# Performance work log

Measured on AMD Instinct MI355X. Metric: run time of the kernel, lower is better.

## Reference

```python
import jax, jax.numpy as jnp
import numpy as np

DIM = 256
HEADS = 8
DIM_FF = 1024
N = 4096
HEAD_DIM = DIM // HEADS
SCALE = HEAD_DIM ** -0.5


def layer_norm(x, gamma, beta, eps=1e-5):
    mu = jnp.mean(x, axis=-1, keepdims=True)
    var = jnp.var(x, axis=-1, keepdims=True)
    return (x - mu) * jax.lax.rsqrt(var + eps) * gamma + beta


def setup_inputs() -> dict:
    key = jax.random.key(0)
    ks = jax.random.split(key, 8)
    x = jax.random.normal(ks[0], (N, DIM), dtype=jnp.float32)
    adj = jax.random.randint(ks[1], (N, N), 0, 2, dtype=jnp.int32)
    adj = adj.at[jnp.arange(N), jnp.arange(N)].set(1)  # self-loops
    s = 1.0 / np.sqrt(DIM)
    w_qkv = jax.random.normal(ks[2], (DIM, 3 * DIM), dtype=jnp.float32) * s
    w_proj = jax.random.normal(ks[3], (DIM, DIM), dtype=jnp.float32) * s
    b_proj = jnp.zeros((DIM,), jnp.float32)
    w1 = jax.random.normal(ks[4], (DIM, DIM_FF), dtype=jnp.float32) * s
    b1 = jnp.zeros((DIM_FF,), jnp.float32)
    w2 = jax.random.normal(ks[5], (DIM_FF, DIM), dtype=jnp.float32) / np.sqrt(DIM_FF)
    b2 = jnp.zeros((DIM,), jnp.float32)
    g1 = jnp.ones((DIM,), jnp.float32)
    be1 = jnp.zeros((DIM,), jnp.float32)
    g2 = jnp.ones((DIM,), jnp.float32)
    be2 = jnp.zeros((DIM,), jnp.float32)
    return {"x": x, "adj": adj, "w_qkv": w_qkv, "w_proj": w_proj,
            "b_proj": b_proj, "w1": w1, "b1": b1, "w2": w2, "b2": b2,
            "g1": g1, "be1": be1, "g2": g2, "be2": be2}


def reference(x, adj, w_qkv, w_proj, b_proj, w1, b1, w2, b2, g1, be1, g2, be2):
    n = x.shape[0]
    qkv = layer_norm(x, g1, be1) @ w_qkv            # (N, 3*dim)
    qkv = qkv.reshape(n, 3, HEADS, HEAD_DIM)
    q, k, v = qkv[:, 0], qkv[:, 1], qkv[:, 2]       # (N, h, d)
    scores = jnp.einsum('nhd,mhd->hnm', q, k) * SCALE
    mask = (adj != 0)[None, :, :]                    # (1, N, N)
    scores = jnp.where(mask, scores, -jnp.inf)
    attn = jax.nn.softmax(scores, axis=-1)           # (h, N, N)
    out = jnp.einsum('hnm,mhd->nhd', attn, v).reshape(n, DIM)
    x = x + out @ w_proj + b_proj
    h2 = layer_norm(x, g2, be2)
    ff = jax.nn.gelu(h2 @ w1 + b1) @ w2 + b2
    return x + ff
```

## Files before the change

### kernel.cpp

```cpp
#include <hip/hip_runtime.h>
#include <hip/hip_bf16.h>

#define NT 4096
#define DM 256
#define NH 8
#define HD 32
#define DFF 1024

typedef __attribute__((ext_vector_type(8))) short s8v;
typedef __attribute__((ext_vector_type(4))) float f4v;
typedef __attribute__((ext_vector_type(2))) float f2v;
typedef __attribute__((ext_vector_type(16))) float f16v;
typedef __attribute__((ext_vector_type(4))) int i4v;

static __device__ __forceinline__ unsigned short f2b(float f){
  union{float f; unsigned u;} v; v.f=f;
  return (unsigned short)((v.u + 0x7FFFu + ((v.u>>16)&1u))>>16);
}

static __device__ __forceinline__ void gl_lds16(const void* g, void* l){
  __builtin_amdgcn_global_load_lds(
      (const __attribute__((address_space(1))) unsigned int*)g,
      (__attribute__((address_space(3))) unsigned int*)l, 16, 0, 0);
}

__global__ __launch_bounds__(256) void prologue_kernel(
    const int* __restrict__ adj, unsigned long long* __restrict__ mask,
    const float* __restrict__ wqkv, const float* __restrict__ wproj,
    const float* __restrict__ w1, const float* __restrict__ w2,
    unsigned short* __restrict__ wqkvT, unsigned short* __restrict__ wprojT,
    unsigned short* __restrict__ w1T, unsigned short* __restrict__ w2T,
    const float* __restrict__ x, const float* __restrict__ g1,
    const float* __restrict__ be1, unsigned short* __restrict__ h1){
  int bx = blockIdx.x;
  if (bx < 1024){
    int wv = threadIdx.x>>6, lane = threadIdx.x&63;
    int base = (bx*4 + wv)*64;
    for (int it=0; it<16; ++it){
      int w0 = base + it*4;
      unsigned long long b0 = __ballot(adj[(long)(w0+0)*64 + lane]!=0);
      unsigned long long b1 = __ballot(adj[(long)(w0+1)*64 + lane]!=0);
      unsigned long long b2 = __ballot(adj[(long)(w0+2)*64 + lane]!=0);
      unsigned long long b3 = __ballot(adj[(long)(w0+3)*64 + lane]!=0);
      if (lane==0){ mask[w0]=b0; mask[w0+1]=b1; mask[w0+2]=b2; mask[w0+3]=b3; }
    }
  } else if (bx < 1152){
    int t = (bx-1024)*256 + threadIdx.x;
    const int stride = 128*256;
    for (int i=t;i<768*DM;i+=stride){int n=i>>8,k=i&255; wqkvT[i]=f2b(wqkv[k*768+n]);}
    for (int i=t;i<DM*DM;i+=stride){int n=i>>8,k=i&255; wprojT[i]=f2b(wproj[k*DM+n]);}
    for (int i=t;i<DFF*DM;i+=stride){int n=i>>8,k=i&255; w1T[i]=f2b(w1[k*DFF+n]);}
    for (int i=t;i<DM*DFF;i+=stride){int n=i/DFF,k=i-n*DFF; w2T[i]=f2b(w2[k*DM+n]);}
  } else {
    int wv = threadIdx.x>>6, lane = threadIdx.x&63;
    int rbase = (bx-1152)*4 + wv;
    for (int j=0;j<8;j++){
      int row = rbase + j*512;
      float4 v = *(const float4*)(x + row*DM + lane*4);
      float s = v.x+v.y+v.z+v.w;
      float sq = v.x*v.x+v.y*v.y+v.z*v.z+v.w*v.w;
      #pragma unroll
      for (int m=1;m<64;m<<=1){ s += __shfl_xor(s,m); sq += __shfl_xor(sq,m); }
      float mu = s*(1.0f/DM);
      float rs = rsqrtf(sq*(1.0f/DM) - mu*mu + 1e-5f);
      float4 gv = *(const float4*)(g1 + lane*4);
      float4 bv = *(const float4*)(be1 + lane*4);
      ushort4 o;
      o.x = f2b((v.x-mu)*rs*gv.x + bv.x);
      o.y = f2b((v.y-mu)*rs*gv.y + bv.y);
      o.z = f2b((v.z-mu)*rs*gv.z + bv.z);
      o.w = f2b((v.w-mu)*rs*gv.w + bv.w);
      *(ushort4*)(h1 + row*DM + lane*4) = o;
    }
  }
}

template<int KD, int MODE>
__global__ __launch_bounds__(256,4) void gemm24(const unsigned short* __restrict__ A,
            const unsigned short* __restrict__ Wt, const float* __restrict__ bias,
            void* __restrict__ outp,
            unsigned short* __restrict__ Qp, unsigned short* __restrict__ Kp,
            unsigned short* __restrict__ Vt){
  int wv = threadIdx.x>>6, lane = threadIdx.x&63;
  int lo = lane&15, hi = lane>>4;
  int r0 = blockIdx.y*32;
  int cbase = blockIdx.x*256 + wv*16;
  const unsigned short* ar0 = A + (r0+lo)*KD + hi*8;
  const unsigned short* ar1 = ar0 + 16*KD;
  const unsigned short* br0 = Wt + (cbase     +lo)*KD + hi*8;
  const unsigned short* br1 = Wt + (cbase+ 64 +lo)*KD + hi*8;
  const unsigned short* br2 = Wt + (cbase+128 +lo)*KD + hi*8;
  const unsigned short* br3 = Wt + (cbase+192 +lo)*KD + hi*8;
  f4v c00={0,0,0,0},c01={0,0,0,0},c02={0,0,0,0},c03={0,0,0,0};
  f4v c10={0,0,0,0},c11={0,0,0,0},c12={0,0,0,0},c13={0,0,0,0};
  #pragma unroll 2
  for (int k0=0;k0<KD;k0+=32){
    s8v a0 = *(const s8v*)(ar0 + k0);
    s8v a1 = *(const s8v*)(ar1 + k0);
    s8v b0 = *(const s8v*)(br0 + k0);
    s8v b1 = *(const s8v*)(br1 + k0);
    s8v b2 = *(const s8v*)(br2 + k0);
    s8v b3 = *(const s8v*)(br3 + k0);
    c00 = __builtin_amdgcn_mfma_f32_16x16x32_bf16(a0,b0,c00,0,0,0);
    c10 = __builtin_amdgcn_mfma_f32_16x16x32_bf16(a1,b0,c10,0,0,0);
    c01 = __builtin_amdgcn_mfma_f32_16x16x32_bf16(a0,b1,c01,0,0,0);
    c11 = __builtin_amdgcn_mfma_f32_16x16x32_bf16(a1,b1,c11,0,0,0);
    c02 = __builtin_amdgcn_mfma_f32_16x16x32_bf16(a0,b2,c02,0,0,0);
    c12 = __builtin_amdgcn_mfma_f32_16x16x32_bf16(a1,b2,c12,0,0,0);
    c03 = __builtin_amdgcn_mfma_f32_16x16x32_bf16(a0,b3,c03,0,0,0);
    c13 = __builtin_amdgcn_mfma_f32_16x16x32_bf16(a1,b3,c13,0,0,0);
  }
  const float scl2 = (float)(0.17677669529663687 * 1.4426950408889634);
  #pragma unroll
  for (int rt=0;rt<2;rt++){
    f4v e0 = rt? c10:c00, e1 = rt? c11:c01, e2 = rt? c12:c02, e3 = rt? c13:c03;
    int nb = r0 + rt*16 + hi*4;
    #pragma unroll
    for (int jj=0;jj<4;jj++){
      f4v acc = jj==0?e0 : jj==1?e1 : jj==2?e2 : e3;
      int c = cbase + jj*64 + lo;
      if (MODE==0){
        int which = c>>8, hd = c&255, hh = hd>>5, d = hd&31;
        #pragma unroll
        for (int r=0;r<4;r++){
          int n = nb + r;
          float val = acc[r];
          if (which==0) Qp[(hh*NT+n)*HD+d]=f2b(val*scl2);
          else if (which==1) Kp[(hh*NT+n)*HD+d]=f2b(val);
          else Vt[(hh*HD+d)*NT+n]=f2b(val);
        }
      }
    }
  }
}

__global__ __launch_bounds__(512,2) void attn_kernel(
    const unsigned short* __restrict__ Q, const unsigned short* __restrict__ K,
    const unsigned short* __restrict__ Vt, const unsigned* __restrict__ mb32,
    unsigned short* __restrict__ out){
  __shared__ float Opart[8][32][34];
  __shared__ float llS[8][32];
  int wv = threadIdx.x>>6, lane = threadIdx.x&63;
  int l31 = lane&31, hi5 = lane>>5;
  int h = blockIdx.x, q0 = blockIdx.y*64;
  const unsigned short* QbA = Q + (h*NT + q0 + l31)*HD + hi5*8;
  const unsigned short* QbB = QbA + 32*HD;
  s8v bqA1 = *(const s8v*)(QbA);
  s8v bqA2 = *(const s8v*)(QbA + 16);
  s8v bqB1 = *(const s8v*)(QbB);
  s8v bqB2 = *(const s8v*)(QbB + 16);
  const unsigned short* Kb = K + h*NT*HD;
  const unsigned short* Vb = Vt + (h*HD + l31)*NT;
  const unsigned* mrowA = mb32 + (q0+l31)*(NT/32) + wv*16;
  const unsigned* mrowB = mrowA + 32*(NT/32);
  const float C0 = -11.541560327111707f;
  const f16v c0v = {C0,C0,C0,C0,C0,C0,C0,C0,C0,C0,C0,C0,C0,C0,C0,C0};
  f2v lacA = {0.f,0.f}, lacB = {0.f,0.f};
  f16v accA = {0,0,0,0,0,0,0,0,0,0,0,0,0,0,0,0};
  f16v accB = {0,0,0,0,0,0,0,0,0,0,0,0,0,0,0,0};
  union SU { f16v v; f2v p[8]; };
  const unsigned short* Kt0 = Kb + (wv*512 + l31)*HD + hi5*8;
  s8v kc1 = *(const s8v*)(Kt0);
  s8v kc2 = *(const s8v*)(Kt0 + 16);
  for (int tg=0; tg<4; tg++){
    i4v mw4A = *(const i4v*)(mrowA + tg*4);
    i4v mw4B = *(const i4v*)(mrowB + tg*4);
    #pragma unroll
    for (int ti=0; ti<4; ti++){
      int t = tg*4 + ti;
      int m0 = wv*512 + t*32;
      const unsigned short* Vtp = Vb + m0 + hi5*8;
      s8v av1 = *(const s8v*)(Vtp);
      s8v av2 = *(const s8v*)(Vtp + 16);
      int tn = (t<15)? t+1 : 15;
      const unsigned short* Ktn = Kb + (wv*512 + tn*32 + l31)*HD + hi5*8;
      s8v kn1 = *(const s8v*)(Ktn);
      s8v kn2 = *(const s8v*)(Ktn + 16);
      SU sa, sb;
      __builtin_amdgcn_s_setprio(1);
      sa.v = __builtin_amdgcn_mfma_f32_32x32x16_bf16(kc1, bqA1, c0v, 0,0,0);
      sa.v = __builtin_amdgcn_mfma_f32_32x32x16_bf16(kc2, bqA2, sa.v, 0,0,0);
      sb.v = __builtin_amdgcn_mfma_f32_32x32x16_bf16(kc1, bqB1, c0v, 0,0,0);
      sb.v = __builtin_amdgcn_mfma_f32_32x32x16_bf16(kc2, bqB2, sb.v, 0,0,0);
      __builtin_amdgcn_s_setprio(0);
      unsigned mwA = ((unsigned)mw4A[ti]) >> (4*hi5);
      unsigned mwB = ((unsigned)mw4B[ti]) >> (4*hi5);
      #pragma unroll
      for (int r=0;r<16;r++){
        int bp = (r&3)+8*(r>>2);
        float pa = __builtin_amdgcn_exp2f(sa.v[r]);
        float pb = __builtin_amdgcn_exp2f(sb.v[r]);
        sa.v[r] = ((mwA >> bp) & 1u) ? pa : 0.0f;
        sb.v[r] = ((mwB >> bp) & 1u) ? pb : 0.0f;
      }
      #pragma unroll
      for (int i=0;i<8;i++){ lacA += sa.p[i]; lacB += sb.p[i]; }
      unsigned a0,a1,a2,a3,a4,a5,a6,a7, b0,b1,b2,b3,b4,b5,b6,b7;
      asm("v_cvt_pk_bf16_f32 %0, %1, %2" : "=v"(a0) : "v"(sa.v[0]),  "v"(sa.v[1]));
      asm("v_cvt_pk_bf16_f32 %0, %1, %2" : "=v"(a1) : "v"(sa.v[2]),  "v"(sa.v[3]));
      asm("v_cvt_pk_bf16_f32 %0, %1, %2" : "=v"(a2) : "v"(sa.v[4]),  "v"(sa.v[5]));
      asm("v_cvt_pk_bf16_f32 %0, %1, %2" : "=v"(a3) : "v"(sa.v[6]),  "v"(sa.v[7]));
      asm("v_cvt_pk_bf16_f32 %0, %1, %2" : "=v"(a4) : "v"(sa.v[8]),  "v"(sa.v[9]));
      asm("v_cvt_pk_bf16_f32 %0, %1, %2" : "=v"(a5) : "v"(sa.v[10]), "v"(sa.v[11]));
      asm("v_cvt_pk_bf16_f32 %0, %1, %2" : "=v"(a6) : "v"(sa.v[12]), "v"(sa.v[13]));
      asm("v_cvt_pk_bf16_f32 %0, %1, %2" : "=v"(a7) : "v"(sa.v[14]), "v"(sa.v[15]));
      asm("v_permlane32_swap_b32 %0, %1" : "+v"(a0), "+v"(a2));
      asm("v_permlane32_swap_b32 %0, %1" : "+v"(a1), "+v"(a3));
      asm("v_permlane32_swap_b32 %0, %1" : "+v"(a4), "+v"(a6));
      asm("v_permlane32_swap_b32 %0, %1" : "+v"(a5), "+v"(a7));
      asm("v_cvt_pk_bf16_f32 %0, %1, %2" : "=v"(b0) : "v"(sb.v[0]),  "v"(sb.v[1]));
      asm("v_cvt_pk_bf16_f32 %0, %1, %2" : "=v"(b1) : "v"(sb.v[2]),  "v"(sb.v[3]));
      asm("v_cvt_pk_bf16_f32 %0, %1, %2" : "=v"(b2) : "v"(sb.v[4]),  "v"(sb.v[5]));
      asm("v_cvt_pk_bf16_f32 %0, %1, %2" : "=v"(b3) : "v"(sb.v[6]),  "v"(sb.v[7]));
      asm("v_cvt_pk_bf16_f32 %0, %1, %2" : "=v"(b4) : "v"(sb.v[8]),  "v"(sb.v[9]));
      asm("v_cvt_pk_bf16_f32 %0, %1, %2" : "=v"(b5) : "v"(sb.v[10]), "v"(sb.v[11]));
      asm("v_cvt_pk_bf16_f32 %0, %1, %2" : "=v"(b6) : "v"(sb.v[12]), "v"(sb.v[13]));
      asm("v_cvt_pk_bf16_f32 %0, %1, %2" : "=v"(b7) : "v"(sb.v[14]), "v"(sb.v[15]));
      asm("v_permlane32_swap_b32 %0, %1" : "+v"(b0), "+v"(b2));
      asm("v_permlane32_swap_b32 %0, %1" : "+v"(b1), "+v"(b3));
      asm("v_permlane32_swap_b32 %0, %1" : "+v"(b4), "+v"(b6));
      asm("v_permlane32_swap_b32 %0, %1" : "+v"(b5), "+v"(b7));
      i4v pA1i = {(int)a0,(int)a1,(int)a2,(int)a3};
      i4v pA2i = {(int)a4,(int)a5,(int)a6,(int)a7};
      i4v pB1i = {(int)b0,(int)b1,(int)b2,(int)b3};
      i4v pB2i = {(int)b4,(int)b5,(int)b6,(int)b7};
      s8v pA1 = __builtin_bit_cast(s8v, pA1i);
      s8v pA2 = __builtin_bit_cast(s8v, pA2i);
      s8v pB1 = __builtin_bit_cast(s8v, pB1i);
      s8v pB2 = __builtin_bit_cast(s8v, pB2i);
      __builtin_amdgcn_s_setprio(1);
      accA = __builtin_amdgcn_mfma_f32_32x32x16_bf16(av1, pA1, accA, 0,0,0);
      accA = __builtin_amdgcn_mfma_f32_32x32x16_bf16(av2, pA2, accA, 0,0,0);
      accB = __builtin_amdgcn_mfma_f32_32x32x16_bf16(av1, pB1, accB, 0,0,0);
      accB = __builtin_amdgcn_mfma_f32_32x32x16_bf16(av2, pB2, accB, 0,0,0);
      __builtin_amdgcn_s_setprio(0);
      kc1 = kn1; kc2 = kn2;
    }
  }
  int tid = threadIdx.x;
  int qq = tid>>4, dd = 2*(tid&15);
  #pragma unroll
  for (int i=0;i<8;i++){
    int d = (2*i&3) + 8*(i>>1) + 4*hi5;
    float2 p2; p2.x = accA[2*i]; p2.y = accA[2*i+1];
    *(float2*)&Opart[wv][l31][d] = p2;
  }
  float lsumA = lacA[0] + lacA[1];
  lsumA += __shfl_xor(lsumA, 32);
  if (hi5==0) llS[wv][l31] = lsumA;
  __syncthreads();
  {
    float L=0.f, o0=0.f, o1=0.f;
    #pragma unroll
    for (int u=0;u<8;u++){
      L  += llS[u][qq];
      o0 += Opart[u][qq][dd];
      o1 += Opart[u][qq][dd+1];
    }
    float inv = 1.0f/L;
    float r0 = o0*inv, r1 = o1*inv;
    unsigned pw;
    asm("v_cvt_pk_bf16_f32 %0, %1, %2" : "=v"(pw) : "v"(r0), "v"(r1));
    *(unsigned*)(out + (q0+qq)*DM + h*HD + dd) = pw;
  }
  __syncthreads();
  #pragma unroll
  for (int i=0;i<8;i++){
    int d = (2*i&3) + 8*(i>>1) + 4*hi5;
    float2 p2; p2.x = accB[2*i]; p2.y = accB[2*i+1];
    *(float2*)&Opart[wv][l31][d] = p2;
  }
  float lsumB = lacB[0] + lacB[1];
  lsumB += __shfl_xor(lsumB, 32);
  if (hi5==0) llS[wv][l31] = lsumB;
  __syncthreads();
  {
    float L=0.f, o0=0.f, o1=0.f;
    #pragma unroll
    for (int u=0;u<8;u++){
      L  += llS[u][qq];
      o0 += Opart[u][qq][dd];
      o1 += Opart[u][qq][dd+1];
    }
    float inv = 1.0f/L;
    float r0 = o0*inv, r1 = o1*inv;
    unsigned pw;
    asm("v_cvt_pk_bf16_f32 %0, %1, %2" : "=v"(pw) : "v"(r0), "v"(r1));
    *(unsigned*)(out + (q0+32+qq)*DM + h*HD + dd) = pw;
  }
}

__global__ __launch_bounds__(512,2) void tail_kernel(
    const unsigned short* __restrict__ ao, const unsigned short* __restrict__ wprojT,
    const float* __restrict__ bproj, const float* __restrict__ x,
    const float* __restrict__ g2, const float* __restrict__ be2,
    const unsigned short* __restrict__ w1T, const float* __restrict__ b1,
    const unsigned short* __restrict__ w2T, const float* __restrict__ b2,
    float* __restrict__ outp){
  __shared__ unsigned short h2L[16][DM];
  __shared__ unsigned short gL[16][DFF];
  __shared__ float Ss[8][16], Sq[8][16];
  __shared__ __align__(16) unsigned char wS[2][32768];
  int wv = threadIdx.x>>6, lane = threadIdx.x&63;
  int lo = lane&15, hi = lane>>4;
  int tid = threadIdx.x;
  int r0 = blockIdx.x*16;
  float t[2][4];

#define STAGE_W1(S_, BUF_)                                                    \
  { int cb_ = (S_)>>2, kt_ = (S_)&3;                                          \
    _Pragma("unroll")                                                         \
    for (int rr=0; rr<4; ++rr){                                               \
      int col_ = cb_*256 + rr*64 + (tid>>3);                                  \
      int ko_  = (tid&7) ^ (col_&7);                                          \
      gl_lds16(w1T + col_*DM + kt_*64 + ko_*8,                                \
               &wS[BUF_][rr*8192 + tid*16]);                                  \
    } }

#define STAGE_W2(KT, BUF)                                                     \
  { _Pragma("unroll")                                                         \
    for (int rr=0; rr<4; ++rr){                                               \
      int col_ = rr*64 + (tid>>3);                                            \
      int ko_  = (tid&7) ^ (col_&7);                                          \
      gl_lds16(w2T + col_*DFF + (KT)*64 + ko_*8,                              \
               &wS[BUF][rr*8192 + tid*16]);                                   \
    } }

  STAGE_W1(0, 0);
  STAGE_W1(1, 1);

  {
    const unsigned short* ar  = ao + (r0+lo)*DM + hi*8;
    const unsigned short* pb0 = wprojT + (wv*16     +lo)*DM + hi*8;
    const unsigned short* pb1 = wprojT + (wv*16+128 +lo)*DM + hi*8;
    f4v a0={0,0,0,0}, a1={0,0,0,0};
    #pragma unroll
    for (int k0=0;k0<DM;k0+=32){
      s8v a = *(const s8v*)(ar + k0);
      a0 = __builtin_amdgcn_mfma_f32_16x16x32_bf16(a, *(const s8v*)(pb0+k0), a0,0,0,0);
      a1 = __builtin_amdgcn_mfma_f32_16x16x32_bf16(a, *(const s8v*)(pb1+k0), a1,0,0,0);
    }
    float sr[4]={0,0,0,0}, sq[4]={0,0,0,0};
    #pragma unroll
    for (int jj=0;jj<2;jj++){
      f4v acc = jj? a1 : a0;
      int c = jj*128 + wv*16 + lo;
      float bc = bproj[c];
      #pragma unroll
      for (int r=0;r<4;r++){
        int n = r0 + hi*4 + r;
        float tv = acc[r] + bc + x[n*DM+c];
        t[jj][r] = tv; sr[r] += tv; sq[r] += tv*tv;
      }
    }
    #pragma unroll
    for (int m=1;m<16;m<<=1){
      #pragma unroll
      for (int r=0;r<4;r++){ sr[r]+=__shfl_xor(sr[r],m); sq[r]+=__shfl_xor(sq[r],m); }
    }
    if (lo==0){
      #pragma unroll
      for (int r=0;r<4;r++){ Ss[wv][hi*4+r]=sr[r]; Sq[wv][hi*4+r]=sq[r]; }
    }
    __syncthreads();
    #pragma unroll
    for (int r=0;r<4;r++){
      int nl = hi*4+r;
      float S=0.f, Qs=0.f;
      #pragma unroll
      for (int u=0;u<8;u++){ S += Ss[u][nl]; Qs += Sq[u][nl]; }
      float mu = S*(1.0f/DM);
      float rs = rsqrtf(Qs*(1.0f/DM) - mu*mu + 1e-5f);
      #pragma unroll
      for (int jj=0;jj<2;jj++){
        int c = jj*128 + wv*16 + lo;
        unsigned short hv = f2b((t[jj][r]-mu)*rs*g2[c] + be2[c]);
        int g = c>>3;
        h2L[nl][((g^(nl&7))<<3) + (c&7)] = hv;
      }
    }
  }
  __syncthreads();

  for (int cb=0; cb<4; ++cb){
    f4v f0={0,0,0,0}, f1={0,0,0,0};
    int c0i = wv*16 + lo;
    int c1i = c0i + 128;
    for (int kt=0; kt<4; ++kt){
      int s = cb*4 + kt;
      if (s>=1 && s<15) STAGE_W1(s+1, (s+1)&1);
      const unsigned char* bufp = wS[s&1];
      #pragma unroll
      for (int ks=0; ks<2; ++ks){
        int k0 = kt*64 + ks*32;
        s8v a  = *(const s8v*)&h2L[lo][(((hi + (k0>>3)) ^ (lo&7))<<3)];
        s8v bw0 = *(const s8v*)(bufp + c0i*128 + ((((ks*4)+hi) ^ (c0i&7))<<4));
        s8v bw1 = *(const s8v*)(bufp + c1i*128 + ((((ks*4)+hi) ^ (c1i&7))<<4));
        f0 = __builtin_amdgcn_mfma_f32_16x16x32_bf16(a, bw0, f0,0,0,0);
        f1 = __builtin_amdgcn_mfma_f32_16x16x32_bf16(a, bw1, f1,0,0,0);
      }
      __syncthreads();
    }
    if (cb==3){ STAGE_W2(0, 0); STAGE_W2(1, 1); }
    #pragma unroll
    for (int jj=0;jj<2;jj++){
      f4v acc = jj? f1 : f0;
      int c = cb*256 + jj*128 + wv*16 + lo;
      float bc = b1[c];
      #pragma unroll
      for (int r=0;r<4;r++){
        int nl = hi*4+r;
        float xx = acc[r] + bc;
        float x2v = xx*xx;
        float arg = xx*(2.302340531f + 0.102952640f*x2v);
        float e  = __builtin_amdgcn_exp2f(arg);
        float rcp = __builtin_amdgcn_rcpf(e + 1.0f);
        unsigned short gv = f2b(xx - xx*rcp);
        int g = c>>3;
        gL[nl][((g^(nl&7))<<3) + (c&7)] = gv;
      }
    }
  }
  __syncthreads();

  {
    f4v e0={0,0,0,0}, e1={0,0,0,0};
    int c0i = wv*16 + lo;
    int c1i = c0i + 128;
    for (int kt=0; kt<16; ++kt){
      if (kt>=1 && kt<15) STAGE_W2(kt+1, (kt+1)&1);
      const unsigned char* bufp = wS[kt&1];
      #pragma unroll
      for (int ks=0; ks<2; ++ks){
        int k0 = kt*64 + ks*32;
        s8v a = *(const s8v*)&gL[lo][(((hi + (k0>>3)) ^ (lo&7))<<3)];
        s8v bw0 = *(const s8v*)(bufp + c0i*128 + ((((ks*4)+hi) ^ (c0i&7))<<4));
        s8v bw1 = *(const s8v*)(bufp + c1i*128 + ((((ks*4)+hi) ^ (c1i&7))<<4));
        e0 = __builtin_amdgcn_mfma_f32_16x16x32_bf16(a, bw0, e0,0,0,0);
        e1 = __builtin_amdgcn_mfma_f32_16x16x32_bf16(a, bw1, e1,0,0,0);
      }
      __syncthreads();
    }
    #pragma unroll
    for (int jj=0;jj<2;jj++){
      f4v acc = jj? e1 : e0;
      int c = jj*128 + wv*16 + lo;
      float bc = b2[c];
      #pragma unroll
      for (int r=0;r<4;r++){
        int n = r0 + hi*4 + r;
        outp[n*DM+c] = acc[r] + bc + t[jj][r];
      }
    }
  }
#undef STAGE_W1
#undef STAGE_W2
}

extern "C" void kernel_launch(void* const* d_in, const int* in_sizes, int n_in,
                              void* d_out, int out_size, void* d_ws, size_t ws_size,
                              hipStream_t stream){
  const float* x     = (const float*)d_in[0];
  const int*   adj   = (const int*)d_in[1];
  const float* wqkv  = (const float*)d_in[2];
  const float* wproj = (const float*)d_in[3];
  const float* bproj = (const float*)d_in[4];
  const float* w1    = (const float*)d_in[5];
  const float* b1    = (const float*)d_in[6];
  const float* w2    = (const float*)d_in[7];
  const float* b2    = (const float*)d_in[8];
  const float* g1    = (const float*)d_in[9];
  const float* be1   = (const float*)d_in[10];
  const float* g2    = (const float*)d_in[11];
  const float* be2   = (const float*)d_in[12];

  char* ws = (char*)d_ws;
  unsigned short* h1    = (unsigned short*)(ws + (0u<<20));
  unsigned short* Qb    = (unsigned short*)(ws + (2u<<20));
  unsigned short* Kb    = (unsigned short*)(ws + (4u<<20));
  unsigned short* Vt    = (unsigned short*)(ws + (6u<<20));
  unsigned short* ao    = (unsigned short*)(ws + (8u<<20));
  unsigned short* wqkvT = (unsigned short*)(ws + (24u<<20));
  unsigned short* wprojT= (unsigned short*)(ws + (25u<<20));
  unsigned short* w1T   = (unsigned short*)(ws + (26u<<20));
  unsigned short* w2T   = (unsigned short*)(ws + (27u<<20));
  unsigned long long* mbits = (unsigned long long*)(ws + (28u<<20));
  float* outF = (float*)d_out;

  hipLaunchKernelGGL(prologue_kernel, dim3(1280), dim3(256), 0, stream,
                     adj, mbits, wqkv, wproj, w1, w2, wqkvT, wprojT, w1T, w2T,
                     x, g1, be1, h1);
  hipLaunchKernelGGL((gemm24<256,0>), dim3(3,128), dim3(256), 0, stream,
                     h1, wqkvT, nullptr, nullptr, Qb, Kb, Vt);
  hipLaunchKernelGGL(attn_kernel, dim3(8,64), dim3(512), 0, stream,
                     Qb, Kb, Vt, (const unsigned*)mbits, ao);
  hipLaunchKernelGGL(tail_kernel, dim3(256), dim3(512), 0, stream,
                     ao, wprojT, bproj, x, g2, be2, w1T, b1, w2T, b2, outF);
}
```

Before: 111.4 us.

## Move mask packing into QKV GEMM launch and deepen tail weight prefetch pipeline

The adjacency-to-bitmask packing moves from the prologue into extra blocks of the QKV GEMM launch, so it overlaps with the matmul instead of running alongside the weight transposes. In the tail kernel, the W1/W2 LDS staging is reorganised so each stage issues the load two steps ahead right after a barrier, and partial vmcnt waits replace full __syncthreads. Bias values are also hoisted into registers. The manual waitcnt and barrier scheme adds the risk of subtle synchronisation errors.

```diff
diff --git a/kernel.cpp b/kernel.cpp
--- a/kernel.cpp
+++ b/kernel.cpp
@@ -25,7 +25,6 @@
 }
 
 __global__ __launch_bounds__(256) void prologue_kernel(
-    const int* __restrict__ adj, unsigned long long* __restrict__ mask,
     const float* __restrict__ wqkv, const float* __restrict__ wproj,
     const float* __restrict__ w1, const float* __restrict__ w2,
     unsigned short* __restrict__ wqkvT, unsigned short* __restrict__ wprojT,
@@ -33,19 +32,8 @@
     const float* __restrict__ x, const float* __restrict__ g1,
     const float* __restrict__ be1, unsigned short* __restrict__ h1){
   int bx = blockIdx.x;
-  if (bx < 1024){
-    int wv = threadIdx.x>>6, lane = threadIdx.x&63;
-    int base = (bx*4 + wv)*64;
-    for (int it=0; it<16; ++it){
-      int w0 = base + it*4;
-      unsigned long long b0 = __ballot(adj[(long)(w0+0)*64 + lane]!=0);
-      unsigned long long b1 = __ballot(adj[(long)(w0+1)*64 + lane]!=0);
-      unsigned long long b2 = __ballot(adj[(long)(w0+2)*64 + lane]!=0);
-      unsigned long long b3 = __ballot(adj[(long)(w0+3)*64 + lane]!=0);
-      if (lane==0){ mask[w0]=b0; mask[w0+1]=b1; mask[w0+2]=b2; mask[w0+3]=b3; }
-    }
-  } else if (bx < 1152){
-    int t = (bx-1024)*256 + threadIdx.x;
+  if (bx < 128){
+    int t = bx*256 + threadIdx.x;
     const int stride = 128*256;
     for (int i=t;i<768*DM;i+=stride){int n=i>>8,k=i&255; wqkvT[i]=f2b(wqkv[k*768+n]);}
     for (int i=t;i<DM*DM;i+=stride){int n=i>>8,k=i&255; wprojT[i]=f2b(wproj[k*DM+n]);}
@@ -53,7 +41,7 @@
     for (int i=t;i<DM*DFF;i+=stride){int n=i/DFF,k=i-n*DFF; w2T[i]=f2b(w2[k*DM+n]);}
   } else {
     int wv = threadIdx.x>>6, lane = threadIdx.x&63;
-    int rbase = (bx-1152)*4 + wv;
+    int rbase = (bx-128)*4 + wv;
     for (int j=0;j<8;j++){
       int row = rbase + j*512;
       float4 v = *(const float4*)(x + row*DM + lane*4);
@@ -77,11 +65,24 @@
 
 template<int KD, int MODE>
 __global__ __launch_bounds__(256,4) void gemm24(const unsigned short* __restrict__ A,
-            const unsigned short* __restrict__ Wt, const float* __restrict__ bias,
-            void* __restrict__ outp,
+            const unsigned short* __restrict__ Wt,
+            const int* __restrict__ adj, unsigned long long* __restrict__ mask,
             unsigned short* __restrict__ Qp, unsigned short* __restrict__ Kp,
             unsigned short* __restrict__ Vt){
   int wv = threadIdx.x>>6, lane = threadIdx.x&63;
+  if (blockIdx.x >= 3){
+    int bxl = (blockIdx.x-3)*128 + blockIdx.y;
+    int base = (bxl*4 + wv)*64;
+    for (int it=0; it<16; ++it){
+      int w0 = base + it*4;
+      unsigned long long b0 = __ballot(adj[(long)(w0+0)*64 + lane]!=0);
+      unsigned long long b1 = __ballot(adj[(long)(w0+1)*64 + lane]!=0);
+      unsigned long long b2 = __ballot(adj[(long)(w0+2)*64 + lane]!=0);
+      unsigned long long b3 = __ballot(adj[(long)(w0+3)*64 + lane]!=0);
+      if (lane==0){ mask[w0]=b0; mask[w0+1]=b1; mask[w0+2]=b2; mask[w0+3]=b3; }
+    }
+    return;
+  }
   int lo = lane&15, hi = lane>>4;
   int r0 = blockIdx.y*32;
   int cbase = blockIdx.x*256 + wv*16;
@@ -119,16 +120,14 @@
     for (int jj=0;jj<4;jj++){
       f4v acc = jj==0?e0 : jj==1?e1 : jj==2?e2 : e3;
       int c = cbase + jj*64 + lo;
-      if (MODE==0){
-        int which = c>>8, hd = c&255, hh = hd>>5, d = hd&31;
-        #pragma unroll
-        for (int r=0;r<4;r++){
-          int n = nb + r;
-          float val = acc[r];
-          if (which==0) Qp[(hh*NT+n)*HD+d]=f2b(val*scl2);
-          else if (which==1) Kp[(hh*NT+n)*HD+d]=f2b(val);
-          else Vt[(hh*HD+d)*NT+n]=f2b(val);
-        }
+      int which = c>>8, hd = c&255, hh = hd>>5, d = hd&31;
+      #pragma unroll
+      for (int r=0;r<4;r++){
+        int n = nb + r;
+        float val = acc[r];
+        if (which==0) Qp[(hh*NT+n)*HD+d]=f2b(val*scl2);
+        else if (which==1) Kp[(hh*NT+n)*HD+d]=f2b(val);
+        else Vt[(hh*HD+d)*NT+n]=f2b(val);
       }
     }
   }
@@ -308,26 +307,35 @@
   float t[2][4];
 
 #define STAGE_W1(S_, BUF_)                                                    \
-  { int cb_ = (S_)>>2, kt_ = (S_)&3;                                          \
+  do { int cb_ = (S_)>>2, kt_ = (S_)&3;                                       \
     _Pragma("unroll")                                                         \
     for (int rr=0; rr<4; ++rr){                                               \
       int col_ = cb_*256 + rr*64 + (tid>>3);                                  \
       int ko_  = (tid&7) ^ (col_&7);                                          \
       gl_lds16(w1T + col_*DM + kt_*64 + ko_*8,                                \
                &wS[BUF_][rr*8192 + tid*16]);                                  \
-    } }
+    } } while(0)
 
 #define STAGE_W2(KT, BUF)                                                     \
-  { _Pragma("unroll")                                                         \
+  do { _Pragma("unroll")                                                      \
     for (int rr=0; rr<4; ++rr){                                               \
       int col_ = rr*64 + (tid>>3);                                            \
       int ko_  = (tid&7) ^ (col_&7);                                          \
       gl_lds16(w2T + col_*DFF + (KT)*64 + ko_*8,                              \
                &wS[BUF][rr*8192 + tid*16]);                                   \
-    } }
+    } } while(0)
 
   STAGE_W1(0, 0);
   STAGE_W1(1, 1);
+
+  float b1r[4][2], b2r[2];
+  #pragma unroll
+  for (int cb=0; cb<4; ++cb){
+    b1r[cb][0] = b1[cb*256 +        wv*16 + lo];
+    b1r[cb][1] = b1[cb*256 + 128 +  wv*16 + lo];
+  }
+  b2r[0] = b2[       wv*16 + lo];
+  b2r[1] = b2[128 +  wv*16 + lo];
 
   {
     const unsigned short* ar  = ao + (r0+lo)*DM + hi*8;
@@ -386,9 +394,9 @@
     f4v f0={0,0,0,0}, f1={0,0,0,0};
     int c0i = wv*16 + lo;
     int c1i = c0i + 128;
+    #pragma unroll
     for (int kt=0; kt<4; ++kt){
       int s = cb*4 + kt;
-      if (s>=1 && s<15) STAGE_W1(s+1, (s+1)&1);
       const unsigned char* bufp = wS[s&1];
       #pragma unroll
       for (int ks=0; ks<2; ++ks){
@@ -399,14 +407,21 @@
         f0 = __builtin_amdgcn_mfma_f32_16x16x32_bf16(a, bw0, f0,0,0,0);
         f1 = __builtin_amdgcn_mfma_f32_16x16x32_bf16(a, bw1, f1,0,0,0);
       }
-      __syncthreads();
-    }
-    if (cb==3){ STAGE_W2(0, 0); STAGE_W2(1, 1); }
+      asm volatile("" ::: "memory");
+      __builtin_amdgcn_s_barrier();
+      if (s <= 13)      { STAGE_W1(s+2, s&1); }
+      else if (s == 14) { STAGE_W2(0, 0); }
+      else              { STAGE_W2(1, 1); }
+      if (s < 15){
+        asm volatile("s_waitcnt vmcnt(4)" ::: "memory");
+        __builtin_amdgcn_s_barrier();
+      }
+    }
     #pragma unroll
     for (int jj=0;jj<2;jj++){
       f4v acc = jj? f1 : f0;
       int c = cb*256 + jj*128 + wv*16 + lo;
-      float bc = b1[c];
+      float bc = b1r[cb][jj];
       #pragma unroll
       for (int r=0;r<4;r++){
         int nl = hi*4+r;
@@ -428,7 +443,6 @@
     int c0i = wv*16 + lo;
     int c1i = c0i + 128;
     for (int kt=0; kt<16; ++kt){
-      if (kt>=1 && kt<15) STAGE_W2(kt+1, (kt+1)&1);
       const unsigned char* bufp = wS[kt&1];
       #pragma unroll
       for (int ks=0; ks<2; ++ks){
@@ -439,13 +453,22 @@
         e0 = __builtin_amdgcn_mfma_f32_16x16x32_bf16(a, bw0, e0,0,0,0);
         e1 = __builtin_amdgcn_mfma_f32_16x16x32_bf16(a, bw1, e1,0,0,0);
       }
-      __syncthreads();
+      asm volatile("" ::: "memory");
+      __builtin_amdgcn_s_barrier();
+      if (kt+2 < 16) { STAGE_W2(kt+2, kt&1); }
+      if (kt <= 13){
+        asm volatile("s_waitcnt vmcnt(4)" ::: "memory");
+        __builtin_amdgcn_s_barrier();
+      } else if (kt == 14){
+        asm volatile("s_waitcnt vmcnt(0)" ::: "memory");
+        __builtin_amdgcn_s_barrier();
+      }
     }
     #pragma unroll
     for (int jj=0;jj<2;jj++){
       f4v acc = jj? e1 : e0;
       int c = jj*128 + wv*16 + lo;
-      float bc = b2[c];
+      float bc = b2r[jj];
       #pragma unroll
       for (int r=0;r<4;r++){
         int n = r0 + hi*4 + r;
@@ -487,11 +510,11 @@
   unsigned long long* mbits = (unsigned long long*)(ws + (28u<<20));
   float* outF = (float*)d_out;
 
-  hipLaunchKernelGGL(prologue_kernel, dim3(1280), dim3(256), 0, stream,
-                     adj, mbits, wqkv, wproj, w1, w2, wqkvT, wprojT, w1T, w2T,
+  hipLaunchKernelGGL(prologue_kernel, dim3(256), dim3(256), 0, stream,
+                     wqkv, wproj, w1, w2, wqkvT, wprojT, w1T, w2T,
                      x, g1, be1, h1);
-  hipLaunchKernelGGL((gemm24<256,0>), dim3(3,128), dim3(256), 0, stream,
-                     h1, wqkvT, nullptr, nullptr, Qb, Kb, Vt);
+  hipLaunchKernelGGL((gemm24<256,0>), dim3(11,128), dim3(256), 0, stream,
+                     h1, wqkvT, adj, mbits, Qb, Kb, Vt);
   hipLaunchKernelGGL(attn_kernel, dim3(8,64), dim3(512), 0, stream,
                      Qb, Kb, Vt, (const unsigned*)mbits, ao);
   hipLaunchKernelGGL(tail_kernel, dim3(256), dim3(512), 0, stream,
```

Result: faster. 99.00 us (-11.1%).
